# Kernel optimization log

Measured on AMD Instinct MI355X. Metric: run time of the kernel, lower is better.

Reference implementation:

```python
import jax, jax.numpy as jnp
import numpy as np

N_USERS = 20000
N_ENTITIES = 80000
N = N_USERS + N_ENTITIES
EMBED_DIM = 128
CONV = [128, 128, 64, 32]  # [embed_dim] + eval(conv_dim_list)
NNZ = 1_600_000
CF_B = 8192
CF_L2_LAMBDA = 1e-5


def setup_inputs() -> dict:
    key = jax.random.key(0)
    ks = jax.random.split(key, 20)
    inp = {}
    inp["embed_table"] = jax.random.normal(ks[0], (N, EMBED_DIM), jnp.float32) * 0.02
    ki = 1
    for l in range(3):
        din, dout = CONV[l], CONV[l + 1]
        s = 1.0 / np.sqrt(din).astype(np.float32)
        inp[f"W1_{l}"] = jax.random.normal(ks[ki], (din, dout), jnp.float32) * s; ki += 1
        inp[f"b1_{l}"] = jnp.zeros((dout,), jnp.float32)
        inp[f"W2_{l}"] = jax.random.normal(ks[ki], (din, dout), jnp.float32) * s; ki += 1
        inp[f"b2_{l}"] = jnp.zeros((dout,), jnp.float32)
    inp["edge_rows"] = jax.random.randint(ks[7], (NNZ,), 0, N, jnp.int32)
    inp["edge_cols"] = jax.random.randint(ks[8], (NNZ,), 0, N, jnp.int32)
    # Laplacian-like normalized attention values (positive, ~1/degree scale)
    inp["edge_vals"] = jax.random.uniform(ks[9], (NNZ,), jnp.float32) / 16.0
    inp["user_ids"] = jax.random.randint(ks[10], (CF_B,), 0, N_USERS, jnp.int32)
    inp["item_pos_ids"] = jax.random.randint(ks[11], (CF_B,), N_USERS, N, jnp.int32)
    inp["item_neg_ids"] = jax.random.randint(ks[12], (CF_B,), N_USERS, N, jnp.int32)
    return inp


def _l2_normalize(x):
    # F.normalize(x, p=2, dim=1): x / max(||x||_2, eps)
    n = jnp.linalg.norm(x, axis=1, keepdims=True)
    return x / jnp.maximum(n, 1e-12)


def _l2_loss_mean(x):
    return jnp.mean(jnp.sum(x * x, axis=1) / 2.0)


def _calc_cf_embeddings(embed_table, layer_params, edge_rows, edge_cols, edge_vals):
    n = embed_table.shape[0]
    ego = embed_table
    outs = [ego]
    for (W1, b1, W2, b2) in layer_params:
        # sparse A @ ego via gather + segment_sum (SpMM in COO form)
        msgs = edge_vals[:, None] * ego[edge_cols]          # [nnz, d_in]
        side = jax.ops.segment_sum(msgs, edge_rows, num_segments=n)  # [n, d_in]
        # bi-interaction aggregator (mess_dropout = 0)
        ego = (jax.nn.leaky_relu((ego + side) @ W1 + b1)
               + jax.nn.leaky_relu((ego * side) @ W2 + b2))
        outs.append(_l2_normalize(ego))
    return jnp.concatenate(outs, axis=1)  # [n, 128+128+64+32]


def reference(embed_table, W1_0, b1_0, W2_0, b2_0, W1_1, b1_1, W2_1, b2_1,
              W1_2, b1_2, W2_2, b2_2, edge_rows, edge_cols, edge_vals,
              user_ids, item_pos_ids, item_neg_ids):
    layer_params = [(W1_0, b1_0, W2_0, b2_0),
                    (W1_1, b1_1, W2_1, b2_1),
                    (W1_2, b1_2, W2_2, b2_2)]
    all_embed = _calc_cf_embeddings(embed_table, layer_params,
                                    edge_rows, edge_cols, edge_vals)
    u = all_embed[user_ids]
    p = all_embed[item_pos_ids]
    ng = all_embed[item_neg_ids]
    pos_score = jnp.sum(u * p, axis=1)
    neg_score = jnp.sum(u * ng, axis=1)
    cf_loss = jnp.mean(-jax.nn.log_sigmoid(pos_score - neg_score))
    l2 = _l2_loss_mean(u) + _l2_loss_mean(p) + _l2_loss_mean(ng)
    return cf_loss + CF_L2_LAMBDA * l2
```

## Files before the change

### kernel.cpp

```cpp
#include <hip/hip_runtime.h>
#include <math.h>

static constexpr int N_NODES = 100000;
static constexpr int NNZ     = 1600000;
static constexpr int CFB     = 8192;
static constexpr int NBUCK   = (N_NODES + 63) / 64;
static constexpr int N4      = N_NODES * 128 / 4;
static constexpr int NCHUNK  = 512;
static constexpr int EPC     = NNZ / NCHUNK;
static constexpr int NE      = NBUCK * NCHUNK;

static constexpr int WOF_10 = 0;
static constexpr int WOF_20 = 16384;
static constexpr int WOF_11 = 32768;
static constexpr int WOF_21 = 40960;
static constexpr int WOF_12 = 49152;
static constexpr int WOF_22 = 51200;
static constexpr int WTOT   = 53248;

typedef short bf16x8 __attribute__((ext_vector_type(8)));
typedef float f32x4  __attribute__((ext_vector_type(4)));
typedef float f32x2  __attribute__((ext_vector_type(2)));

__device__ __forceinline__ float lrelu(float x) { return x >= 0.0f ? x : 0.01f * x; }

__device__ __forceinline__ unsigned short f2bf(float x) {
  unsigned u = __float_as_uint(x);
  u += 0x7FFFu + ((u >> 16) & 1u);
  return (unsigned short)(u >> 16);
}
__device__ __forceinline__ float bf2f(unsigned short h) {
  return __uint_as_float(((unsigned)h) << 16);
}
__device__ __forceinline__ unsigned pack2(float x, float y) {
  return (unsigned)f2bf(x) | ((unsigned)f2bf(y) << 16);
}

__global__ __launch_bounds__(256)
void cvt_fused(const float* __restrict__ embed, unsigned short* __restrict__ e0,
               unsigned char* __restrict__ q0,
               const float* __restrict__ W1_0, const float* __restrict__ W2_0,
               const float* __restrict__ W1_1, const float* __restrict__ W2_1,
               const float* __restrict__ W1_2, const float* __restrict__ W2_2,
               unsigned short* __restrict__ wt,
               const int* __restrict__ erows, int* __restrict__ cnt) {
  __shared__ int h[NBUCK];
  for (int b = threadIdx.x; b < NBUCK; b += 256) h[b] = 0;
  __syncthreads();
  const int c = blockIdx.x;
  const int e0i = c * EPC, e1i = e0i + EPC;
  for (int i = e0i + threadIdx.x; i < e1i; i += 256)
    atomicAdd(&h[erows[i] >> 6], 1);
  __syncthreads();
  for (int b = threadIdx.x; b < NBUCK; b += 256)
    cnt[c * NBUCK + b] = h[b];

  const int gid    = blockIdx.x * 256 + threadIdx.x;
  const int stride = NCHUNK * 256;
  for (int i = gid; i < N4; i += stride) {
    float4 v = reinterpret_cast<const float4*>(embed)[i];
    uint2 o; o.x = pack2(v.x, v.y); o.y = pack2(v.z, v.w);
    reinterpret_cast<uint2*>(e0)[i] = o;
    int q = __builtin_amdgcn_cvt_pk_fp8_f32(v.x * 1024.f, v.y * 1024.f, 0, false);
    q = __builtin_amdgcn_cvt_pk_fp8_f32(v.z * 1024.f, v.w * 1024.f, q, true);
    reinterpret_cast<unsigned*>(q0)[i] = (unsigned)q;
  }
  for (int i = gid; i < WTOT; i += stride) {
    const float* src; int off, din, dout;
    if      (i < WOF_20) { src = W1_0; off = WOF_10; din = 128; dout = 128; }
    else if (i < WOF_11) { src = W2_0; off = WOF_20; din = 128; dout = 128; }
    else if (i < WOF_21) { src = W1_1; off = WOF_11; din = 128; dout = 64;  }
    else if (i < WOF_12) { src = W2_1; off = WOF_21; din = 128; dout = 64;  }
    else if (i < WOF_22) { src = W1_2; off = WOF_12; din = 64;  dout = 32;  }
    else                 { src = W2_2; off = WOF_22; din = 64;  dout = 32;  }
    int j = i - off;
    int cc = j / din;
    int k  = j % din;
    wt[i] = f2bf(src[(size_t)k * dout + cc]);
  }
}

__global__ __launch_bounds__(512)
void bucket_scan(int* __restrict__ cnt, int* __restrict__ btot) {
  __shared__ int s[NCHUNK];
  const int b = blockIdx.x;
  const int t = threadIdx.x;
  int v = cnt[(size_t)t * NBUCK + b];
  s[t] = v;
  __syncthreads();
  for (int off = 1; off < NCHUNK; off <<= 1) {
    int x = (t >= off) ? s[t - off] : 0;
    __syncthreads();
    s[t] += x;
    __syncthreads();
  }
  cnt[(size_t)t * NBUCK + b] = s[t] - v;
  if (t == NCHUNK - 1) btot[b] = s[t];
}

__global__ __launch_bounds__(256)
void base_scan(const int* __restrict__ btot, int* __restrict__ bbase) {
  __shared__ int tsum[256];
  const int t = threadIdx.x;
  int loc[8];
  int s = 0;
  #pragma unroll
  for (int j = 0; j < 8; ++j) {
    int idx = t * 8 + j;
    int v = (idx < NBUCK) ? btot[idx] : 0;
    loc[j] = s; s += v;
  }
  tsum[t] = s;
  __syncthreads();
  for (int off = 1; off < 256; off <<= 1) {
    int v = (t >= off) ? tsum[t - off] : 0;
    __syncthreads();
    tsum[t] += v;
    __syncthreads();
  }
  int base = (t == 0) ? 0 : tsum[t - 1];
  #pragma unroll
  for (int j = 0; j < 8; ++j) {
    int idx = t * 8 + j;
    if (idx < NBUCK) bbase[idx] = base + loc[j];
  }
  if (t == 0) bbase[NBUCK] = NNZ;
}

__global__ __launch_bounds__(256)
void scatter_bucket(const int* __restrict__ erows, const int* __restrict__ ecols,
                    const float* __restrict__ evals, const int* __restrict__ cnt,
                    const int* __restrict__ bbase, uint2* __restrict__ spackA) {
  __shared__ int cur[NBUCK];
  const int c = blockIdx.x;
  for (int b = threadIdx.x; b < NBUCK; b += 256)
    cur[b] = bbase[b] + cnt[c * NBUCK + b];
  __syncthreads();
  const int e0 = c * EPC, e1 = e0 + EPC;
  for (int i = e0 + threadIdx.x; i < e1; i += 256) {
    int r = erows[i];
    int p = atomicAdd(&cur[r >> 6], 1);
    uint2 rec;
    rec.x = (unsigned)ecols[i] | ((unsigned)(r & 63) << 17);
    rec.y = __float_as_uint(evals[i]);
    spackA[p] = rec;
  }
}

__global__ __launch_bounds__(256)
void bucket_sort(const int* __restrict__ bbase, const uint2* __restrict__ spackA,
                 uint2* __restrict__ spackB, int* __restrict__ row_ptr) {
  __shared__ int hist[64];
  __shared__ int hcur[64];
  const int b = blockIdx.x;
  const int tid = threadIdx.x;
  const int j0 = bbase[b], j1 = bbase[b + 1];
  if (tid < 64) hist[tid] = 0;
  __syncthreads();
  for (int k = j0 + tid; k < j1; k += 256)
    atomicAdd(&hist[(spackA[k].x >> 17) & 63], 1);
  __syncthreads();
  if (tid == 0) {
    int s = 0, row0 = b * 64;
    for (int r = 0; r < 64; ++r) {
      int v = hist[r];
      hcur[r] = s;
      if (row0 + r < N_NODES) row_ptr[row0 + r] = j0 + s;
      s += v;
    }
    if (b == NBUCK - 1) row_ptr[N_NODES] = NNZ;
  }
  __syncthreads();
  for (int k = j0 + tid; k < j1; k += 256) {
    uint2 rec = spackA[k];
    int rl = (rec.x >> 17) & 63;
    int p = j0 + atomicAdd(&hcur[rl], 1);
    spackB[p] = rec;
  }
}

template<int DIN>
__global__ __launch_bounds__(256)
void spmm_fp8(const unsigned char* __restrict__ qtab, float inv_scale,
              const int* __restrict__ row_ptr,
              const uint2* __restrict__ spack,
              unsigned short* __restrict__ side) {
  int row  = blockIdx.x * 4 + (threadIdx.x >> 6);
  int lane = threadIdx.x & 63;
  if (row >= N_NODES) return;
  int j0 = row_ptr[row], j1 = row_ptr[row + 1];
  if constexpr (DIN == 128) {
    float ax = 0.f, ay = 0.f;
    #pragma unroll 8
    for (int j = j0; j < j1; ++j) {
      uint2 rec = spack[j];
      float v = __uint_as_float(rec.y);
      unsigned q = *reinterpret_cast<const unsigned short*>(
          qtab + (size_t)(rec.x & 0x1FFFF) * 128 + lane * 2);
      f32x2 xy = __builtin_amdgcn_cvt_pk_f32_fp8(q, false);
      ax += v * xy.x;  ay += v * xy.y;
    }
    *reinterpret_cast<unsigned*>(side + (size_t)row * 128 + lane * 2) =
        pack2(ax * inv_scale, ay * inv_scale);
  } else {
    const int half = lane >> 5;
    const int hl   = lane & 31;
    float ax = 0.f, ay = 0.f;
    #pragma unroll 8
    for (int j = j0 + half; j < j1; j += 2) {
      uint2 rec = spack[j];
      float v = __uint_as_float(rec.y);
      unsigned q = *reinterpret_cast<const unsigned short*>(
          qtab + (size_t)(rec.x & 0x1FFFF) * 64 + hl * 2);
      f32x2 xy = __builtin_amdgcn_cvt_pk_f32_fp8(q, false);
      ax += v * xy.x;  ay += v * xy.y;
    }
    ax += __shfl_xor(ax, 32);
    ay += __shfl_xor(ay, 32);
    if (lane < 32)
      *reinterpret_cast<unsigned*>(side + (size_t)row * 64 + hl * 2) =
          pack2(ax * inv_scale, ay * inv_scale);
  }
}

template<int DIN, int DOUT, int WM, int WN, int TPB, bool QOUT>
__global__ __launch_bounds__(256)
void bi_mfma(const unsigned short* __restrict__ ego,
             const unsigned short* __restrict__ side,
             const unsigned short* __restrict__ W1t, const float* __restrict__ b1,
             const unsigned short* __restrict__ W2t, const float* __restrict__ b2,
             unsigned short* __restrict__ out,
             unsigned char* __restrict__ outq, float qs) {
  static_assert(WM * WN == 4, "4 waves");
  constexpr int KFRAG = DIN / 32;
  constexpr int NCOLS = DOUT / WN;
  constexpr int NFRAG = NCOLS / 16;
  constexpr int MROWS = 32 / WM;
  constexpr int MFRAG = MROWS / 16;
  constexpr int CPR   = DIN / 8;
  constexpr int CHUNKS = 32 * CPR;

  __shared__ __align__(16) unsigned short lds1[32 * DIN];
  __shared__ __align__(16) unsigned short lds2[32 * DIN];

  const int tid  = threadIdx.x;
  const int wid  = tid >> 6;
  const int lane = tid & 63;
  const int n0   = (wid % WN) * NCOLS;
  const int mrow0 = (wid / WN) * MROWS;
  const int lr   = lane & 15;
  const int lk   = (lane >> 4) * 8;

  bf16x8 w1f[KFRAG][NFRAG], w2f[KFRAG][NFRAG];
  #pragma unroll
  for (int kf = 0; kf < KFRAG; ++kf)
    #pragma unroll
    for (int nf = 0; nf < NFRAG; ++nf) {
      int col = n0 + nf * 16 + lr;
      int kr  = kf * 32 + lk;
      w1f[kf][nf] = *reinterpret_cast<const bf16x8*>(W1t + (size_t)col * DIN + kr);
      w2f[kf][nf] = *reinterpret_cast<const bf16x8*>(W2t + (size_t)col * DIN + kr);
    }
  float b1v[NFRAG], b2v[NFRAG];
  #pragma unroll
  for (int nf = 0; nf < NFRAG; ++nf) {
    b1v[nf] = b1[n0 + nf * 16 + lr];
    b2v[nf] = b2[n0 + nf * 16 + lr];
  }

  for (int t = 0; t < TPB; ++t) {
    int row0 = (blockIdx.x * TPB + t) * 32;
    if (row0 >= N_NODES) break;
    __syncthreads();
    for (int ci = tid; ci < CHUNKS; ci += 256) {
      int r  = ci / CPR;
      int c8 = ci % CPR;
      size_t g = (size_t)(row0 + r) * DIN + c8 * 8;
      uint4 e4 = *reinterpret_cast<const uint4*>(ego + g);
      uint4 s4 = *reinterpret_cast<const uint4*>(side + g);
      uint4 h1v, h2v;
      {
        float ex, ey, sx, sy;
        ex = bf2f((unsigned short)(e4.x & 0xFFFFu)); ey = bf2f((unsigned short)(e4.x >> 16));
        sx = bf2f((unsigned short)(s4.x & 0xFFFFu)); sy = bf2f((unsigned short)(s4.x >> 16));
        h1v.x = pack2(ex + sx, ey + sy); h2v.x = pack2(ex * sx, ey * sy);
        ex = bf2f((unsigned short)(e4.y & 0xFFFFu)); ey = bf2f((unsigned short)(e4.y >> 16));
        sx = bf2f((unsigned short)(s4.y & 0xFFFFu)); sy = bf2f((unsigned short)(s4.y >> 16));
        h1v.y = pack2(ex + sx, ey + sy); h2v.y = pack2(ex * sx, ey * sy);
        ex = bf2f((unsigned short)(e4.z & 0xFFFFu)); ey = bf2f((unsigned short)(e4.z >> 16));
        sx = bf2f((unsigned short)(s4.z & 0xFFFFu)); sy = bf2f((unsigned short)(s4.z >> 16));
        h1v.z = pack2(ex + sx, ey + sy); h2v.z = pack2(ex * sx, ey * sy);
        ex = bf2f((unsigned short)(e4.w & 0xFFFFu)); ey = bf2f((unsigned short)(e4.w >> 16));
        sx = bf2f((unsigned short)(s4.w & 0xFFFFu)); sy = bf2f((unsigned short)(s4.w >> 16));
        h1v.w = pack2(ex + sx, ey + sy); h2v.w = pack2(ex * sx, ey * sy);
      }
      unsigned byte = ((unsigned)(r * DIN + c8 * 8)) * 2u;
      byte ^= (unsigned)((r & 7) << 4);
      *reinterpret_cast<uint4*>(reinterpret_cast<char*>(lds1) + byte) = h1v;
      *reinterpret_cast<uint4*>(reinterpret_cast<char*>(lds2) + byte) = h2v;
    }
    __syncthreads();

    f32x4 acc1[MFRAG][NFRAG], acc2[MFRAG][NFRAG];
    #pragma unroll
    for (int mf = 0; mf < MFRAG; ++mf)
      #pragma unroll
      for (int nf = 0; nf < NFRAG; ++nf) {
        acc1[mf][nf] = (f32x4)0.f;
        acc2[mf][nf] = (f32x4)0.f;
      }
    #pragma unroll
    for (int kf = 0; kf < KFRAG; ++kf) {
      bf16x8 a1[MFRAG], a2[MFRAG];
      #pragma unroll
      for (int mf = 0; mf < MFRAG; ++mf) {
        int r = mrow0 + mf * 16 + lr;
        unsigned byte = ((unsigned)(r * DIN + kf * 32 + lk)) * 2u;
        byte ^= (unsigned)((r & 7) << 4);
        a1[mf] = *reinterpret_cast<const bf16x8*>(reinterpret_cast<const char*>(lds1) + byte);
        a2[mf] = *reinterpret_cast<const bf16x8*>(reinterpret_cast<const char*>(lds2) + byte);
      }
      #pragma unroll
      for (int mf = 0; mf < MFRAG; ++mf)
        #pragma unroll
        for (int nf = 0; nf < NFRAG; ++nf) {
          acc1[mf][nf] = __builtin_amdgcn_mfma_f32_16x16x32_bf16(a1[mf], w1f[kf][nf], acc1[mf][nf], 0, 0, 0);
          acc2[mf][nf] = __builtin_amdgcn_mfma_f32_16x16x32_bf16(a2[mf], w2f[kf][nf], acc2[mf][nf], 0, 0, 0);
        }
    }

    #pragma unroll
    for (int mf = 0; mf < MFRAG; ++mf)
      #pragma unroll
      for (int nf = 0; nf < NFRAG; ++nf) {
        #pragma unroll
        for (int reg = 0; reg < 4; ++reg) {
          int r = row0 + mrow0 + mf * 16 + (lane >> 4) * 4 + reg;
          int c = n0 + nf * 16 + lr;
          float o = lrelu(acc1[mf][nf][reg] + b1v[nf]) + lrelu(acc2[mf][nf][reg] + b2v[nf]);
          out[(size_t)r * DOUT + c] = f2bf(o);
          if constexpr (QOUT) {
            float oq = o * qs;
            outq[(size_t)r * DOUT + c] =
                (unsigned char)(__builtin_amdgcn_cvt_pk_fp8_f32(oq, oq, 0, false) & 0xFF);
          }
        }
      }
  }
}

__global__ __launch_bounds__(256)
void score_all(const float* __restrict__ emb0,
               const unsigned short* __restrict__ e1,
               const unsigned short* __restrict__ e2,
               const unsigned short* __restrict__ e3,
               const int* __restrict__ uid, const int* __restrict__ pid,
               const int* __restrict__ nid,
               float* __restrict__ pos, float* __restrict__ neg,
               float* __restrict__ l2) {
  int i = blockIdx.x * 4 + (threadIdx.x >> 6);
  int lane = threadIdx.x & 63;
  if (i >= CFB) return;
  const int ui = uid[i], pi = pid[i], gi = nid[i];
  float PS = 0.f, NS = 0.f, L2 = 0.f;

  {
    float up = 0, un = 0, uu = 0, pp = 0, nn = 0;
    for (int d = lane; d < 128; d += 64) {
      float a = emb0[(size_t)ui * 128 + d];
      float b = emb0[(size_t)pi * 128 + d];
      float c = emb0[(size_t)gi * 128 + d];
      up += a * b; un += a * c; uu += a * a; pp += b * b; nn += c * c;
    }
    #pragma unroll
    for (int off = 32; off > 0; off >>= 1) {
      up += __shfl_xor(up, off); un += __shfl_xor(un, off);
      uu += __shfl_xor(uu, off); pp += __shfl_xor(pp, off); nn += __shfl_xor(nn, off);
    }
    PS += up; NS += un; L2 += uu + pp + nn;
  }
  const unsigned short* tabs[3] = { e1, e2, e3 };
  const int dims[3] = { 128, 64, 32 };
  #pragma unroll
  for (int L = 0; L < 3; ++L) {
    const unsigned short* T = tabs[L];
    const int dim = dims[L];
    float up = 0, un = 0, uu = 0, pp = 0, nn = 0;
    for (int d = lane; d < dim; d += 64) {
      float a = bf2f(T[(size_t)ui * dim + d]);
      float b = bf2f(T[(size_t)pi * dim + d]);
      float c = bf2f(T[(size_t)gi * dim + d]);
      up += a * b; un += a * c; uu += a * a; pp += b * b; nn += c * c;
    }
    #pragma unroll
    for (int off = 32; off > 0; off >>= 1) {
      up += __shfl_xor(up, off); un += __shfl_xor(un, off);
      uu += __shfl_xor(uu, off); pp += __shfl_xor(pp, off); nn += __shfl_xor(nn, off);
    }
    float mu = fmaxf(sqrtf(uu), 1e-12f);
    float mp = fmaxf(sqrtf(pp), 1e-12f);
    float mn = fmaxf(sqrtf(nn), 1e-12f);
    PS += up / (mu * mp);
    NS += un / (mu * mn);
    L2 += uu / (mu * mu) + pp / (mp * mp) + nn / (mn * mn);
  }
  if (lane == 0) { pos[i] = PS; neg[i] = NS; l2[i] = L2; }
}

__global__ __launch_bounds__(256)
void loss_kernel(const float* __restrict__ pos, const float* __restrict__ neg,
                 const float* __restrict__ l2, float* __restrict__ out) {
  __shared__ float s1[256];
  __shared__ float s2[256];
  int tid = threadIdx.x;
  float cf = 0.f, reg = 0.f;
  for (int i = tid; i < CFB; i += 256) {
    float x = pos[i] - neg[i];
    float sp = (x > 0.f) ? log1pf(expf(-x)) : (-x + log1pf(expf(x)));
    cf  += sp;
    reg += l2[i];
  }
  s1[tid] = cf; s2[tid] = reg;
  __syncthreads();
  for (int s = 128; s > 0; s >>= 1) {
    if (tid < s) { s1[tid] += s1[tid + s]; s2[tid] += s2[tid + s]; }
    __syncthreads();
  }
  if (tid == 0)
    out[0] = s1[0] / (float)CFB + 1e-5f * (0.5f * s2[0] / (float)CFB);
}

extern "C" void kernel_launch(void* const* d_in, const int* in_sizes, int n_in,
                              void* d_out, int out_size, void* d_ws, size_t ws_size,
                              hipStream_t stream) {
  const float* embed = (const float*)d_in[0];
  const float* W1_0 = (const float*)d_in[1];
  const float* b1_0 = (const float*)d_in[2];
  const float* W2_0 = (const float*)d_in[3];
  const float* b2_0 = (const float*)d_in[4];
  const float* W1_1 = (const float*)d_in[5];
  const float* b1_1 = (const float*)d_in[6];
  const float* W2_1 = (const float*)d_in[7];
  const float* b2_1 = (const float*)d_in[8];
  const float* W1_2 = (const float*)d_in[9];
  const float* b1_2 = (const float*)d_in[10];
  const float* W2_2 = (const float*)d_in[11];
  const float* b2_2 = (const float*)d_in[12];
  const int*   erows = (const int*)d_in[13];
  const int*   ecols = (const int*)d_in[14];
  const float* evals = (const float*)d_in[15];
  const int*   uid = (const int*)d_in[16];
  const int*   pid = (const int*)d_in[17];
  const int*   nid = (const int*)d_in[18];

  unsigned short* e0 = (unsigned short*)d_ws;
  unsigned short* e1 = e0 + (size_t)N_NODES * 128;
  unsigned short* e2 = e1 + (size_t)N_NODES * 128;
  unsigned short* e3 = e2 + (size_t)N_NODES * 64;
  unsigned short* sb = e3 + (size_t)N_NODES * 32;
  unsigned char*  q0 = (unsigned char*)(sb + (size_t)N_NODES * 128);
  unsigned char*  q2 = q0 + (size_t)N_NODES * 128;
  unsigned short* wt = (unsigned short*)(q2 + (size_t)N_NODES * 64);
  int*   cnt     = (int*)(wt + WTOT);
  int*   btot    = cnt + NE;
  int*   bbase   = btot + NBUCK;
  int*   row_ptr = bbase + NBUCK + 1;
  uint2* spackA  = (uint2*)(row_ptr + N_NODES + 2);
  uint2* spackB  = spackA + NNZ;
  unsigned char* q1 = (unsigned char*)spackA;
  float* posb    = (float*)(spackB + NNZ);
  float* negb    = posb + CFB;
  float* l2b     = negb + CFB;

  cvt_fused<<<NCHUNK, 256, 0, stream>>>(embed, e0, q0, W1_0, W2_0, W1_1, W2_1,
                                        W1_2, W2_2, wt, erows, cnt);
  bucket_scan<<<NBUCK, NCHUNK, 0, stream>>>(cnt, btot);
  base_scan<<<1, 256, 0, stream>>>(btot, bbase);
  scatter_bucket<<<NCHUNK, 256, 0, stream>>>(erows, ecols, evals, cnt, bbase, spackA);
  bucket_sort<<<NBUCK, 256, 0, stream>>>(bbase, spackA, spackB, row_ptr);

  constexpr int TPB = 5;
  constexpr int GB  = (N_NODES / 32 + TPB - 1) / TPB;

  spmm_fp8<128><<<(N_NODES + 3) / 4, 256, 0, stream>>>(q0, 1.f / 1024.f, row_ptr, spackB, sb);
  bi_mfma<128, 128, 1, 4, TPB, true><<<GB, 256, 0, stream>>>(e0, sb, wt + WOF_10, b1_0, wt + WOF_20, b2_0, e1, q1, 64.f);

  spmm_fp8<128><<<(N_NODES + 3) / 4, 256, 0, stream>>>(q1, 1.f / 64.f, row_ptr, spackB, sb);
  bi_mfma<128, 64, 1, 4, TPB, true><<<GB, 256, 0, stream>>>(e1, sb, wt + WOF_11, b1_1, wt + WOF_21, b2_1, e2, q2, 64.f);

  spmm_fp8<64><<<(N_NODES + 3) / 4, 256, 0, stream>>>(q2, 1.f / 64.f, row_ptr, spackB, sb);
  bi_mfma<64, 32, 2, 2, TPB, false><<<GB, 256, 0, stream>>>(e2, sb, wt + WOF_12, b1_2, wt + WOF_22, b2_2, e3, (unsigned char*)nullptr, 0.f);

  score_all<<<CFB / 4, 256, 0, stream>>>(embed, e1, e2, e3, uid, pid, nid, posb, negb, l2b);
  loss_kernel<<<1, 256, 0, stream>>>(posb, negb, l2b, (float*)d_out);
}
```

Before: 376.2 us.

## Fuse SpMM gather into bi-interaction MFMA kernel per 32-row tile

Combines the per-row FP8 SpMM and the bi-interaction MFMA layer into one kernel. Each wave gathers the neighbours for 8 rows, adds and multiplies them with ego, and writes the results straight into swizzled LDS before the MFMA stage. This drops the bf16 side buffer round-trip through global memory and three kernel launches. In exchange, each block now reloads its weight fragments for only 32 rows instead of five 32-row tiles, and the MFMA phase cannot overlap with gather latency inside a block.

```diff
diff --git a/kernel.cpp b/kernel.cpp
--- a/kernel.cpp
+++ b/kernel.cpp
@@ -179,66 +179,21 @@
   }
 }
 
-template<int DIN>
-__global__ __launch_bounds__(256)
-void spmm_fp8(const unsigned char* __restrict__ qtab, float inv_scale,
-              const int* __restrict__ row_ptr,
-              const uint2* __restrict__ spack,
-              unsigned short* __restrict__ side) {
-  int row  = blockIdx.x * 4 + (threadIdx.x >> 6);
-  int lane = threadIdx.x & 63;
-  if (row >= N_NODES) return;
-  int j0 = row_ptr[row], j1 = row_ptr[row + 1];
-  if constexpr (DIN == 128) {
-    float ax = 0.f, ay = 0.f;
-    #pragma unroll 8
-    for (int j = j0; j < j1; ++j) {
-      uint2 rec = spack[j];
-      float v = __uint_as_float(rec.y);
-      unsigned q = *reinterpret_cast<const unsigned short*>(
-          qtab + (size_t)(rec.x & 0x1FFFF) * 128 + lane * 2);
-      f32x2 xy = __builtin_amdgcn_cvt_pk_f32_fp8(q, false);
-      ax += v * xy.x;  ay += v * xy.y;
-    }
-    *reinterpret_cast<unsigned*>(side + (size_t)row * 128 + lane * 2) =
-        pack2(ax * inv_scale, ay * inv_scale);
-  } else {
-    const int half = lane >> 5;
-    const int hl   = lane & 31;
-    float ax = 0.f, ay = 0.f;
-    #pragma unroll 8
-    for (int j = j0 + half; j < j1; j += 2) {
-      uint2 rec = spack[j];
-      float v = __uint_as_float(rec.y);
-      unsigned q = *reinterpret_cast<const unsigned short*>(
-          qtab + (size_t)(rec.x & 0x1FFFF) * 64 + hl * 2);
-      f32x2 xy = __builtin_amdgcn_cvt_pk_f32_fp8(q, false);
-      ax += v * xy.x;  ay += v * xy.y;
-    }
-    ax += __shfl_xor(ax, 32);
-    ay += __shfl_xor(ay, 32);
-    if (lane < 32)
-      *reinterpret_cast<unsigned*>(side + (size_t)row * 64 + hl * 2) =
-          pack2(ax * inv_scale, ay * inv_scale);
-  }
-}
-
-template<int DIN, int DOUT, int WM, int WN, int TPB, bool QOUT>
-__global__ __launch_bounds__(256)
-void bi_mfma(const unsigned short* __restrict__ ego,
-             const unsigned short* __restrict__ side,
-             const unsigned short* __restrict__ W1t, const float* __restrict__ b1,
-             const unsigned short* __restrict__ W2t, const float* __restrict__ b2,
-             unsigned short* __restrict__ out,
-             unsigned char* __restrict__ outq, float qs) {
+template<int DIN, int DOUT, int WM, int WN, bool QOUT>
+__global__ __launch_bounds__(256)
+void bi_fused(const unsigned char* __restrict__ qtab, float inv_scale,
+              const int* __restrict__ row_ptr, const uint2* __restrict__ spack,
+              const unsigned short* __restrict__ ego,
+              const unsigned short* __restrict__ W1t, const float* __restrict__ b1,
+              const unsigned short* __restrict__ W2t, const float* __restrict__ b2,
+              unsigned short* __restrict__ out,
+              unsigned char* __restrict__ outq, float qs) {
   static_assert(WM * WN == 4, "4 waves");
   constexpr int KFRAG = DIN / 32;
   constexpr int NCOLS = DOUT / WN;
   constexpr int NFRAG = NCOLS / 16;
   constexpr int MROWS = 32 / WM;
   constexpr int MFRAG = MROWS / 16;
-  constexpr int CPR   = DIN / 8;
-  constexpr int CHUNKS = 32 * CPR;
 
   __shared__ __align__(16) unsigned short lds1[32 * DIN];
   __shared__ __align__(16) unsigned short lds2[32 * DIN];
@@ -250,6 +205,7 @@
   const int mrow0 = (wid / WN) * MROWS;
   const int lr   = lane & 15;
   const int lk   = (lane >> 4) * 8;
+  const int row0 = blockIdx.x * 32;
 
   bf16x8 w1f[KFRAG][NFRAG], w2f[KFRAG][NFRAG];
   #pragma unroll
@@ -268,85 +224,104 @@
     b2v[nf] = b2[n0 + nf * 16 + lr];
   }
 
-  for (int t = 0; t < TPB; ++t) {
-    int row0 = (blockIdx.x * TPB + t) * 32;
-    if (row0 >= N_NODES) break;
-    __syncthreads();
-    for (int ci = tid; ci < CHUNKS; ci += 256) {
-      int r  = ci / CPR;
-      int c8 = ci % CPR;
-      size_t g = (size_t)(row0 + r) * DIN + c8 * 8;
-      uint4 e4 = *reinterpret_cast<const uint4*>(ego + g);
-      uint4 s4 = *reinterpret_cast<const uint4*>(side + g);
-      uint4 h1v, h2v;
-      {
-        float ex, ey, sx, sy;
-        ex = bf2f((unsigned short)(e4.x & 0xFFFFu)); ey = bf2f((unsigned short)(e4.x >> 16));
-        sx = bf2f((unsigned short)(s4.x & 0xFFFFu)); sy = bf2f((unsigned short)(s4.x >> 16));
-        h1v.x = pack2(ex + sx, ey + sy); h2v.x = pack2(ex * sx, ey * sy);
-        ex = bf2f((unsigned short)(e4.y & 0xFFFFu)); ey = bf2f((unsigned short)(e4.y >> 16));
-        sx = bf2f((unsigned short)(s4.y & 0xFFFFu)); sy = bf2f((unsigned short)(s4.y >> 16));
-        h1v.y = pack2(ex + sx, ey + sy); h2v.y = pack2(ex * sx, ey * sy);
-        ex = bf2f((unsigned short)(e4.z & 0xFFFFu)); ey = bf2f((unsigned short)(e4.z >> 16));
-        sx = bf2f((unsigned short)(s4.z & 0xFFFFu)); sy = bf2f((unsigned short)(s4.z >> 16));
-        h1v.z = pack2(ex + sx, ey + sy); h2v.z = pack2(ex * sx, ey * sy);
-        ex = bf2f((unsigned short)(e4.w & 0xFFFFu)); ey = bf2f((unsigned short)(e4.w >> 16));
-        sx = bf2f((unsigned short)(s4.w & 0xFFFFu)); sy = bf2f((unsigned short)(s4.w >> 16));
-        h1v.w = pack2(ex + sx, ey + sy); h2v.w = pack2(ex * sx, ey * sy);
+  #pragma unroll
+  for (int rr = 0; rr < 8; ++rr) {
+    const int r   = wid * 8 + rr;
+    const int row = row0 + r;
+    const int j0 = row_ptr[row], j1 = row_ptr[row + 1];
+    if constexpr (DIN == 128) {
+      float ax = 0.f, ay = 0.f;
+      #pragma unroll 8
+      for (int j = j0; j < j1; ++j) {
+        uint2 rec = spack[j];
+        float v = __uint_as_float(rec.y);
+        unsigned q = *reinterpret_cast<const unsigned short*>(
+            qtab + (size_t)(rec.x & 0x1FFFF) * 128 + lane * 2);
+        f32x2 xy = __builtin_amdgcn_cvt_pk_f32_fp8(q, false);
+        ax += v * xy.x;  ay += v * xy.y;
       }
-      unsigned byte = ((unsigned)(r * DIN + c8 * 8)) * 2u;
+      unsigned ev = *reinterpret_cast<const unsigned*>(ego + (size_t)row * 128 + lane * 2);
+      float ex = bf2f((unsigned short)(ev & 0xFFFFu));
+      float ey = bf2f((unsigned short)(ev >> 16));
+      float sx = ax * inv_scale, sy = ay * inv_scale;
+      unsigned byte = ((unsigned)(r * DIN + lane * 2)) * 2u;
       byte ^= (unsigned)((r & 7) << 4);
-      *reinterpret_cast<uint4*>(reinterpret_cast<char*>(lds1) + byte) = h1v;
-      *reinterpret_cast<uint4*>(reinterpret_cast<char*>(lds2) + byte) = h2v;
-    }
-    __syncthreads();
-
-    f32x4 acc1[MFRAG][NFRAG], acc2[MFRAG][NFRAG];
+      *reinterpret_cast<unsigned*>(reinterpret_cast<char*>(lds1) + byte) = pack2(ex + sx, ey + sy);
+      *reinterpret_cast<unsigned*>(reinterpret_cast<char*>(lds2) + byte) = pack2(ex * sx, ey * sy);
+    } else {
+      const int half = lane >> 5;
+      const int hl   = lane & 31;
+      float ax = 0.f, ay = 0.f;
+      #pragma unroll 8
+      for (int j = j0 + half; j < j1; j += 2) {
+        uint2 rec = spack[j];
+        float v = __uint_as_float(rec.y);
+        unsigned q = *reinterpret_cast<const unsigned short*>(
+            qtab + (size_t)(rec.x & 0x1FFFF) * 64 + hl * 2);
+        f32x2 xy = __builtin_amdgcn_cvt_pk_f32_fp8(q, false);
+        ax += v * xy.x;  ay += v * xy.y;
+      }
+      ax += __shfl_xor(ax, 32);
+      ay += __shfl_xor(ay, 32);
+      if (lane < 32) {
+        unsigned ev = *reinterpret_cast<const unsigned*>(ego + (size_t)row * 64 + hl * 2);
+        float ex = bf2f((unsigned short)(ev & 0xFFFFu));
+        float ey = bf2f((unsigned short)(ev >> 16));
+        float sx = ax * inv_scale, sy = ay * inv_scale;
+        unsigned byte = ((unsigned)(r * DIN + hl * 2)) * 2u;
+        byte ^= (unsigned)((r & 7) << 4);
+        *reinterpret_cast<unsigned*>(reinterpret_cast<char*>(lds1) + byte) = pack2(ex + sx, ey + sy);
+        *reinterpret_cast<unsigned*>(reinterpret_cast<char*>(lds2) + byte) = pack2(ex * sx, ey * sy);
+      }
+    }
+  }
+  __syncthreads();
+
+  f32x4 acc1[MFRAG][NFRAG], acc2[MFRAG][NFRAG];
+  #pragma unroll
+  for (int mf = 0; mf < MFRAG; ++mf)
+    #pragma unroll
+    for (int nf = 0; nf < NFRAG; ++nf) {
+      acc1[mf][nf] = (f32x4)0.f;
+      acc2[mf][nf] = (f32x4)0.f;
+    }
+  #pragma unroll
+  for (int kf = 0; kf < KFRAG; ++kf) {
+    bf16x8 a1[MFRAG], a2[MFRAG];
+    #pragma unroll
+    for (int mf = 0; mf < MFRAG; ++mf) {
+      int r = mrow0 + mf * 16 + lr;
+      unsigned byte = ((unsigned)(r * DIN + kf * 32 + lk)) * 2u;
+      byte ^= (unsigned)((r & 7) << 4);
+      a1[mf] = *reinterpret_cast<const bf16x8*>(reinterpret_cast<const char*>(lds1) + byte);
+      a2[mf] = *reinterpret_cast<const bf16x8*>(reinterpret_cast<const char*>(lds2) + byte);
+    }
     #pragma unroll
     for (int mf = 0; mf < MFRAG; ++mf)
       #pragma unroll
       for (int nf = 0; nf < NFRAG; ++nf) {
-        acc1[mf][nf] = (f32x4)0.f;
-        acc2[mf][nf] = (f32x4)0.f;
+        acc1[mf][nf] = __builtin_amdgcn_mfma_f32_16x16x32_bf16(a1[mf], w1f[kf][nf], acc1[mf][nf], 0, 0, 0);
+        acc2[mf][nf] = __builtin_amdgcn_mfma_f32_16x16x32_bf16(a2[mf], w2f[kf][nf], acc2[mf][nf], 0, 0, 0);
       }
-    #pragma unroll
-    for (int kf = 0; kf < KFRAG; ++kf) {
-      bf16x8 a1[MFRAG], a2[MFRAG];
+  }
+
+  #pragma unroll
+  for (int mf = 0; mf < MFRAG; ++mf)
+    #pragma unroll
+    for (int nf = 0; nf < NFRAG; ++nf) {
       #pragma unroll
-      for (int mf = 0; mf < MFRAG; ++mf) {
-        int r = mrow0 + mf * 16 + lr;
-        unsigned byte = ((unsigned)(r * DIN + kf * 32 + lk)) * 2u;
-        byte ^= (unsigned)((r & 7) << 4);
-        a1[mf] = *reinterpret_cast<const bf16x8*>(reinterpret_cast<const char*>(lds1) + byte);
-        a2[mf] = *reinterpret_cast<const bf16x8*>(reinterpret_cast<const char*>(lds2) + byte);
-      }
-      #pragma unroll
-      for (int mf = 0; mf < MFRAG; ++mf)
-        #pragma unroll
-        for (int nf = 0; nf < NFRAG; ++nf) {
-          acc1[mf][nf] = __builtin_amdgcn_mfma_f32_16x16x32_bf16(a1[mf], w1f[kf][nf], acc1[mf][nf], 0, 0, 0);
-          acc2[mf][nf] = __builtin_amdgcn_mfma_f32_16x16x32_bf16(a2[mf], w2f[kf][nf], acc2[mf][nf], 0, 0, 0);
-        }
-    }
-
-    #pragma unroll
-    for (int mf = 0; mf < MFRAG; ++mf)
-      #pragma unroll
-      for (int nf = 0; nf < NFRAG; ++nf) {
-        #pragma unroll
-        for (int reg = 0; reg < 4; ++reg) {
-          int r = row0 + mrow0 + mf * 16 + (lane >> 4) * 4 + reg;
-          int c = n0 + nf * 16 + lr;
-          float o = lrelu(acc1[mf][nf][reg] + b1v[nf]) + lrelu(acc2[mf][nf][reg] + b2v[nf]);
-          out[(size_t)r * DOUT + c] = f2bf(o);
-          if constexpr (QOUT) {
-            float oq = o * qs;
-            outq[(size_t)r * DOUT + c] =
-                (unsigned char)(__builtin_amdgcn_cvt_pk_fp8_f32(oq, oq, 0, false) & 0xFF);
-          }
+      for (int reg = 0; reg < 4; ++reg) {
+        int r = row0 + mrow0 + mf * 16 + (lane >> 4) * 4 + reg;
+        int c = n0 + nf * 16 + lr;
+        float o = lrelu(acc1[mf][nf][reg] + b1v[nf]) + lrelu(acc2[mf][nf][reg] + b2v[nf]);
+        out[(size_t)r * DOUT + c] = f2bf(o);
+        if constexpr (QOUT) {
+          float oq = o * qs;
+          outq[(size_t)r * DOUT + c] =
+              (unsigned char)(__builtin_amdgcn_cvt_pk_fp8_f32(oq, oq, 0, false) & 0xFF);
         }
       }
-  }
+    }
 }
 
 __global__ __launch_bounds__(256)
@@ -457,8 +432,7 @@
   unsigned short* e1 = e0 + (size_t)N_NODES * 128;
   unsigned short* e2 = e1 + (size_t)N_NODES * 128;
   unsigned short* e3 = e2 + (size_t)N_NODES * 64;
-  unsigned short* sb = e3 + (size_t)N_NODES * 32;
-  unsigned char*  q0 = (unsigned char*)(sb + (size_t)N_NODES * 128);
+  unsigned char*  q0 = (unsigned char*)(e3 + (size_t)N_NODES * 32);
   unsigned char*  q2 = q0 + (size_t)N_NODES * 128;
   unsigned short* wt = (unsigned short*)(q2 + (size_t)N_NODES * 64);
   int*   cnt     = (int*)(wt + WTOT);
@@ -479,17 +453,17 @@
   scatter_bucket<<<NCHUNK, 256, 0, stream>>>(erows, ecols, evals, cnt, bbase, spackA);
   bucket_sort<<<NBUCK, 256, 0, stream>>>(bbase, spackA, spackB, row_ptr);
 
-  constexpr int TPB = 5;
-  constexpr int GB  = (N_NODES / 32 + TPB - 1) / TPB;
-
-  spmm_fp8<128><<<(N_NODES + 3) / 4, 256, 0, stream>>>(q0, 1.f / 1024.f, row_ptr, spackB, sb);
-  bi_mfma<128, 128, 1, 4, TPB, true><<<GB, 256, 0, stream>>>(e0, sb, wt + WOF_10, b1_0, wt + WOF_20, b2_0, e1, q1, 64.f);
-
-  spmm_fp8<128><<<(N_NODES + 3) / 4, 256, 0, stream>>>(q1, 1.f / 64.f, row_ptr, spackB, sb);
-  bi_mfma<128, 64, 1, 4, TPB, true><<<GB, 256, 0, stream>>>(e1, sb, wt + WOF_11, b1_1, wt + WOF_21, b2_1, e2, q2, 64.f);
-
-  spmm_fp8<64><<<(N_NODES + 3) / 4, 256, 0, stream>>>(q2, 1.f / 64.f, row_ptr, spackB, sb);
-  bi_mfma<64, 32, 2, 2, TPB, false><<<GB, 256, 0, stream>>>(e2, sb, wt + WOF_12, b1_2, wt + WOF_22, b2_2, e3, (unsigned char*)nullptr, 0.f);
+  constexpr int GB = N_NODES / 32;
+
+  bi_fused<128, 128, 1, 4, true><<<GB, 256, 0, stream>>>(
+      q0, 1.f / 1024.f, row_ptr, spackB, e0, wt + WOF_10, b1_0, wt + WOF_20, b2_0, e1, q1, 64.f);
+
+  bi_fused<128, 64, 1, 4, true><<<GB, 256, 0, stream>>>(
+      q1, 1.f / 64.f, row_ptr, spackB, e1, wt + WOF_11, b1_1, wt + WOF_21, b2_1, e2, q2, 64.f);
+
+  bi_fused<64, 32, 2, 2, false><<<GB, 256, 0, stream>>>(
+      q2, 1.f / 64.f, row_ptr, spackB, e2, wt + WOF_12, b1_2, wt + WOF_22, b2_2, e3,
+      (unsigned char*)nullptr, 0.f);
 
   score_all<<<CFB / 4, 256, 0, stream>>>(embed, e1, e2, e3, uid, pid, nid, posb, negb, l2b);
   loss_kernel<<<1, 256, 0, stream>>>(posb, negb, l2b, (float*)d_out);
```

Result: slower. 527.5 us (+40.2%).
